# Optimization experiments

Hardware: AMD Instinct MI355X
Metric: run time of the kernel (lower is better)

## Reference

```python
import jax, jax.numpy as jnp
import numpy as np

B, T, N, H, D = 4, 512, 4, 8, 64
FACTOR = 5


def setup_inputs() -> dict:
    key = jax.random.key(0)
    k1, k2, k3, k4 = jax.random.split(key, 4)
    queries = jax.random.normal(k1, (B, T, N, H, D), dtype=jnp.float32)
    keys = jax.random.normal(k2, (B, T, N, H, D), dtype=jnp.float32)
    values = jax.random.normal(k3, (B, T, N, H, D), dtype=jnp.float32)
    sample_k = min(FACTOR * int(np.ceil(np.log(T))), T)  # = 35
    index_sample = jax.random.randint(k4, (T, sample_k), 0, T)
    return {"queries": queries, "keys": keys, "values": values,
            "index_sample": index_sample}


def _merge_heads(x):
    # [B, T, N, H, D] -> [B, H, T, N*D]  (matches transpose(3,2).reshape.transpose(2,1))
    b, t, n, h, d = x.shape
    return jnp.transpose(x, (0, 1, 3, 2, 4)).reshape(b, t, h, n * d).transpose(0, 2, 1, 3)


def reference(queries, keys, values, index_sample):
    b, t, n, h, d = queries.shape
    e = n * d
    Q = _merge_heads(queries)   # [B, H, T, E]
    K = _merge_heads(keys)
    V = _merge_heads(values)
    u = index_sample.shape[1]   # sample_k == n_top == factor*ceil(ln T)

    # --- _prob_QK: sampled QK scores, sparsity measure, top-u query select ---
    K_sample = K[:, :, index_sample, :]                      # [B, H, T, u, E]
    QK_sample = jnp.einsum('bhte,bhtse->bhts', Q, K_sample)  # [B, H, T, u]
    M = QK_sample.max(axis=-1) - QK_sample.sum(axis=-1) / t  # [B, H, T]
    _, M_top = jax.lax.top_k(M, u)                           # [B, H, u]
    Q_reduce = jnp.take_along_axis(Q, M_top[..., None], axis=2)  # [B, H, u, E]
    scores = jnp.einsum('bhue,bhte->bhut', Q_reduce, K)      # [B, H, u, T]

    # scale uses 1/sqrt(d_k) of the ORIGINAL query last dim (D), not N*D
    scores = scores * (1.0 / jnp.sqrt(jnp.asarray(d, scores.dtype)))

    # --- initial context (mask_flag=False): mean of V broadcast over T ---
    context = jnp.broadcast_to(V.mean(axis=2, keepdims=True), (b, h, t, e))

    # --- update context at selected query positions ---
    attn = jax.nn.softmax(scores, axis=-1)                   # [B, H, u, T]
    update = jnp.einsum('bhut,bhte->bhue', attn, V)          # [B, H, u, E]
    bi = jnp.arange(b)[:, None, None]
    hi = jnp.arange(h)[None, :, None]
    context = context.at[bi, hi, M_top].set(update)          # scatter-write

    # [B, H, T, E] -> [B, T, N, H, D]
    out = context.transpose(0, 2, 1, 3).reshape(b, t, h, n, d).transpose(0, 1, 3, 2, 4)
    return out
```

## Files before the change

kernel.cpp:

```cpp
#include <hip/hip_runtime.h>
#include <stdint.h>

#define BB 4
#define TT 512
#define NN 4
#define HH 8
#define DD 64
#define EE 256
#define ROWS 2048
#define UPAD 36
#define NCH 8
#define CH 64


__global__ __launch_bounds__(256)
void m_vmean_kernel(const float* __restrict__ q, const float* __restrict__ k,
                    const float* __restrict__ v, const int* __restrict__ idx,
                    float* __restrict__ M, float* __restrict__ vpart, int U) {
    if (blockIdx.x >= 4096) {
        int blk = blockIdx.x - 4096;
        int chunk = blk & 7, bh = blk >> 3;
        int b = bh >> 3, h = bh & 7;
        int e = threadIdx.x;
        int n = e >> 6, d = e & 63;
        size_t base = (size_t)b * TT * ROWS + (size_t)(n * HH + h) * DD + d;
        float acc = 0.f;
        int t0 = chunk * 64;
        for (int t = t0; t < t0 + 64; ++t)
            acc += v[base + (size_t)t * ROWS];
        vpart[blk * EE + e] = acc;
        return;
    }
    __shared__ int sidx[4][40];
    int wave = threadIdx.x >> 6, lane = threadIdx.x & 63;
    int xcd = blockIdx.x & 7;
    int bh = (xcd << 2) | ((blockIdx.x >> 3) & 3);
    int t = ((blockIdx.x >> 5) << 2) + wave;
    int b = bh >> 3, h = bh & 7;
    if (lane < U) sidx[wave][lane] = idx[t * U + lane] & (TT - 1);
    int g = lane >> 4, x = lane & 15;
    int n = x >> 2;
    int dbase = (x & 3) << 4;
    size_t colbase = (size_t)(n * HH + h) * DD + dbase;
    const float* qr = q + ((size_t)(b * TT + t)) * ROWS + colbase;
    float4 qv0 = *(const float4*)qr;
    float4 qv1 = *(const float4*)(qr + 4);
    float4 qv2 = *(const float4*)(qr + 8);
    float4 qv3 = *(const float4*)(qr + 12);
    float mx = -3.4e38f, sm = 0.f;
    const int NB = (U + 3) >> 2;
    int sP = g; if (sP >= U) sP = U - 1;
    const float* kr = k + ((size_t)(b * TT + sidx[wave][sP])) * ROWS + colbase;
    float4 c0 = *(const float4*)kr,       c1 = *(const float4*)(kr + 4),
           c2 = *(const float4*)(kr + 8), c3 = *(const float4*)(kr + 12);
    for (int bs = 0; bs < NB; ++bs) {
        int sn = ((bs + 1) << 2) + g;
        if (sn >= U) sn = U - 1;
        const float* krn = k + ((size_t)(b * TT + sidx[wave][sn])) * ROWS + colbase;
        float4 n0 = *(const float4*)krn,       n1 = *(const float4*)(krn + 4),
               n2 = *(const float4*)(krn + 8), n3 = *(const float4*)(krn + 12);
        float dot = qv0.x * c0.x + qv0.y * c0.y + qv0.z * c0.z + qv0.w * c0.w
                  + qv1.x * c1.x + qv1.y * c1.y + qv1.z * c1.z + qv1.w * c1.w
                  + qv2.x * c2.x + qv2.y * c2.y + qv2.z * c2.z + qv2.w * c2.w
                  + qv3.x * c3.x + qv3.y * c3.y + qv3.z * c3.z + qv3.w * c3.w;
        #pragma unroll
        for (int off = 1; off < 16; off <<= 1)
            dot += __shfl_xor(dot, off, 64);
        int s = (bs << 2) + g;
        if (s < U) { mx = fmaxf(mx, dot); sm += dot; }
        c0 = n0; c1 = n1; c2 = n2; c3 = n3;
    }
    mx = fmaxf(mx, __shfl_xor(mx, 16, 64));
    mx = fmaxf(mx, __shfl_xor(mx, 32, 64));
    sm += __shfl_xor(sm, 16, 64);
    sm += __shfl_xor(sm, 32, 64);
    if (lane == 0) M[(bh << 9) + t] = mx - sm * (1.0f / TT);
}

__global__ void topk_kernel(const float* __restrict__ M,
                            int* __restrict__ Mtop,
                            const float* __restrict__ vpart,
                            float* __restrict__ vmean, int U) {
    __shared__ float sM[TT];
    int bh = blockIdx.x;
    int t = threadIdx.x;
    sM[t] = M[bh * TT + t];
    if (t < 64) Mtop[bh * 64 + t] = 0;
    if (t < EE) {
        float acc = 0.f;
        #pragma unroll
        for (int c = 0; c < 8; ++c)
            acc += vpart[(bh * 8 + c) * EE + t];
        vmean[bh * EE + t] = acc * (1.0f / TT);
    }
    __syncthreads();
    float mv = sM[t];
    int rank = 0;
    for (int i = 0; i < TT; ++i) {
        float o = sM[i];
        rank += (o > mv) || (o == mv && i < t);
    }
    if (rank < U) Mtop[bh * 64 + rank] = t;
}

__global__ __launch_bounds__(256)
void attn_fill(const float* __restrict__ q, const float* __restrict__ k,
               const float* __restrict__ v, const int* __restrict__ Mtop,
               const float* __restrict__ vmean, float* __restrict__ out,
               float* __restrict__ Opart, float* __restrict__ ml, int U) {
    __shared__ float qs[UPAD * 130];
    __shared__ float Bs[CH * 132];
    __shared__ float S[UPAD * 68];

    if (blockIdx.x >= 256) {
        int fb = blockIdx.x - 256;
        size_t i0 = (size_t)fb * 256 + threadIdx.x;
        #pragma unroll
        for (int r = 0; r < 8; ++r) {
            size_t tid4 = (i0 + (size_t)r * 131072) << 2;
            int d = tid4 & 63;
            size_t rest = tid4 >> 6;
            int h = rest & 7;  rest >>= 3;
            int nn = rest & 3; rest >>= 2;
            int b = (int)(rest >> 9);
            int e = (nn << 6) + d;
            int bh = (b << 3) + h;
            float4 val = *(const float4*)(vmean + (size_t)bh * EE + e);
            *(float4*)(out + tid4) = val;
        }
        return;
    }

    int bx = blockIdx.x;
    int bh = bx >> 3, ch = bx & 7;
    int b = bh >> 3, h = bh & 7;
    int tid = threadIdx.x;
    int wv = tid >> 6, l = tid & 63;

    float acc[4][4];
    #pragma unroll
    for (int i = 0; i < 4; ++i)
        #pragma unroll
        for (int j = 0; j < 4; ++j) acc[i][j] = 0.f;

    for (int h2 = 0; h2 < 2; ++h2) {
        int eb = h2 * 128;
        for (int u = wv; u < UPAD; u += 4) {
            int uu = (u < U) ? u : (U - 1);
            int qt = Mtop[bh * 64 + uu] & (TT - 1);
            size_t rowq = ((size_t)(b * TT + qt)) * ROWS;
            #pragma unroll
            for (int j = 0; j < 2; ++j) {
                int e = eb + l + 64 * j;
                qs[u * 130 + l + 64 * j] = q[rowq + (size_t)((e >> 6) * HH + h) * DD + (e & 63)];
            }
        }
        for (int r = wv; r < CH; r += 4) {
            size_t rowk = ((size_t)(b * TT + ch * CH + r)) * ROWS;
            #pragma unroll
            for (int j = 0; j < 2; ++j) {
                int e = eb + l + 64 * j;
                Bs[r * 129 + l + 64 * j] = k[rowk + (size_t)((e >> 6) * HH + h) * DD + (e & 63)];
            }
        }
        __syncthreads();
        if (tid < 144) {
            int ug = tid >> 4, tg = tid & 15;
            int u0 = ug << 2, t0 = tg << 2;
            for (int e = 0; e < 128; ++e) {
                float kx0 = Bs[(t0 + 0) * 129 + e];
                float kx1 = Bs[(t0 + 1) * 129 + e];
                float kx2 = Bs[(t0 + 2) * 129 + e];
                float kx3 = Bs[(t0 + 3) * 129 + e];
                #pragma unroll
                for (int i = 0; i < 4; ++i) {
                    float qv = qs[(u0 + i) * 130 + e];
                    acc[i][0] += qv * kx0;
                    acc[i][1] += qv * kx1;
                    acc[i][2] += qv * kx2;
                    acc[i][3] += qv * kx3;
                }
            }
        }
        __syncthreads();
    }
    if (tid < 144) {
        int ug = tid >> 4, tg = tid & 15;
        int u0 = ug << 2, t0 = tg << 2;
        #pragma unroll
        for (int i = 0; i < 4; ++i)
            #pragma unroll
            for (int j = 0; j < 4; ++j)
                S[(u0 + i) * 68 + t0 + j] = acc[i][j] * 0.125f;
    }
    __syncthreads();

    if (tid < UPAD) {
        float m = -3.4e38f;
        for (int t = 0; t < CH; ++t) m = fmaxf(m, S[tid * 68 + t]);
        float lsum = 0.f;
        for (int t = 0; t < CH; ++t) {
            float p = __expf(S[tid * 68 + t] - m);
            S[tid * 68 + t] = p;
            lsum += p;
        }
        size_t mli = ((size_t)(bh * NCH + ch) * UPAD + tid) * 2;
        ml[mli] = m;
        ml[mli + 1] = lsum;
    }
    __syncthreads();

    int ugp = tid >> 5, el = tid & 31;
    int u0p = ugp * 5;
    for (int vh = 0; vh < 2; ++vh) {
        for (int r = wv; r < CH; r += 4) {
            size_t rowv = ((size_t)(b * TT + ch * CH + r)) * ROWS;
            #pragma unroll
            for (int j = 0; j < 2; ++j) {
                int e = vh * 128 + l + 64 * j;
                Bs[r * 132 + l + 64 * j] = v[rowv + (size_t)((e >> 6) * HH + h) * DD + (e & 63)];
            }
        }
        __syncthreads();
        float4 o[5];
        #pragma unroll
        for (int i = 0; i < 5; ++i) o[i] = make_float4(0.f, 0.f, 0.f, 0.f);
        for (int t = 0; t < CH; ++t) {
            float4 v4 = *(const float4*)&Bs[t * 132 + 4 * el];
            #pragma unroll
            for (int i = 0; i < 5; ++i) {
                int uc = u0p + i; if (uc > 35) uc = 35;
                float p = S[uc * 68 + t];
                o[i].x += p * v4.x; o[i].y += p * v4.y;
                o[i].z += p * v4.z; o[i].w += p * v4.w;
            }
        }
        #pragma unroll
        for (int i = 0; i < 5; ++i) {
            int u = u0p + i;
            if (u < UPAD)
                *(float4*)&Opart[((size_t)(bh * NCH + ch) * UPAD + u) * EE + vh * 128 + 4 * el] = o[i];
        }
        __syncthreads();
    }
}

__global__ void combine_kernel(const float* __restrict__ Opart,
                               const float* __restrict__ ml,
                               const int* __restrict__ Mtop,
                               float* __restrict__ out, int U) {
    int bx = blockIdx.x;
    int bh = bx / U, ui = bx % U;
    int b = bh >> 3, h = bh & 7;
    int el = threadIdx.x;
    float mc[NCH], lc[NCH];
    float gm = -3.4e38f;
    #pragma unroll
    for (int c = 0; c < NCH; ++c) {
        size_t mli = ((size_t)(bh * NCH + c) * UPAD + ui) * 2;
        mc[c] = ml[mli]; lc[c] = ml[mli + 1];
        gm = fmaxf(gm, mc[c]);
    }
    float L = 0.f;
    float fc[NCH];
    #pragma unroll
    for (int c = 0; c < NCH; ++c) { fc[c] = __expf(mc[c] - gm); L += lc[c] * fc[c]; }
    float inv = 1.0f / L;
    float4 a = make_float4(0.f, 0.f, 0.f, 0.f);
    #pragma unroll
    for (int c = 0; c < NCH; ++c) {
        float4 o = *(const float4*)&Opart[((size_t)(bh * NCH + c) * UPAD + ui) * EE + 4 * el];
        a.x += fc[c] * o.x; a.y += fc[c] * o.y;
        a.z += fc[c] * o.z; a.w += fc[c] * o.w;
    }
    int qt = Mtop[bh * 64 + ui] & (TT - 1);
    int e0 = 4 * el, n = el >> 4;
    size_t ooff = ((size_t)(b * TT + qt)) * ROWS + (size_t)(n * HH + h) * DD + (e0 & 63);
    a.x *= inv; a.y *= inv; a.z *= inv; a.w *= inv;
    *(float4*)(out + ooff) = a;
}


__global__ __launch_bounds__(1024)
void vmean_kernel(const float* __restrict__ v, float* __restrict__ vmean) {
    __shared__ float part[4][EE];
    int bh = blockIdx.x;
    int b = bh >> 3, h = bh & 7;
    int e = threadIdx.x & 255;
    int chunk = threadIdx.x >> 8;
    int n = e >> 6, d = e & 63;
    size_t base = (size_t)b * TT * ROWS + (size_t)(n * HH + h) * DD + d;
    float acc = 0.f;
    int t0 = chunk * 128;
    for (int t = t0; t < t0 + 128; ++t)
        acc += v[base + (size_t)t * ROWS];
    part[chunk][e] = acc;
    __syncthreads();
    if (threadIdx.x < EE)
        vmean[bh * EE + threadIdx.x] =
            (part[0][threadIdx.x] + part[1][threadIdx.x] +
             part[2][threadIdx.x] + part[3][threadIdx.x]) * (1.0f / TT);
}

__global__ void fill_kernel(const float* __restrict__ vmean,
                            float* __restrict__ out) {
    size_t tid4 = ((size_t)blockIdx.x * 256 + threadIdx.x) << 2;
    int d = tid4 & 63;
    size_t rest = tid4 >> 6;
    int h = rest & 7;  rest >>= 3;
    int n = rest & 3;  rest >>= 2;
    int b = (int)(rest >> 9);
    int e = (n << 6) + d;
    int bh = (b << 3) + h;
    float4 val = *(const float4*)(vmean + (size_t)bh * EE + e);
    *(float4*)(out + tid4) = val;
}

__global__ void m_only_kernel(const float* __restrict__ q,
                              const float* __restrict__ k,
                              const int* __restrict__ idx,
                              float* __restrict__ M, int U) {
    int wave = threadIdx.x >> 6, lane = threadIdx.x & 63;
    int r = (blockIdx.x << 2) + wave;
    int t = r & (TT - 1);
    int bh = r >> 9;
    int b = bh >> 3, h = bh & 7;
    int g = lane >> 4, x = lane & 15;
    int n = x >> 2;
    int dbase = (x & 3) << 4;
    size_t colbase = (size_t)(n * HH + h) * DD + dbase;
    size_t qrow = ((size_t)(b * TT + t)) * ROWS + colbase;
    float4 qv0 = *(const float4*)(q + qrow);
    float4 qv1 = *(const float4*)(q + qrow + 4);
    float4 qv2 = *(const float4*)(q + qrow + 8);
    float4 qv3 = *(const float4*)(q + qrow + 12);
    float mx = -3.4e38f, sm = 0.f;
    int NB = (U + 3) >> 2;
    for (int bs = 0; bs < NB; ++bs) {
        int s = (bs << 2) + g;
        int valid = s < U;
        int sc = valid ? s : (U - 1);
        int kt = idx[t * U + sc] & (TT - 1);
        size_t krow = ((size_t)(b * TT + kt)) * ROWS + colbase;
        float4 kv0 = *(const float4*)(k + krow);
        float4 kv1 = *(const float4*)(k + krow + 4);
        float4 kv2 = *(const float4*)(k + krow + 8);
        float4 kv3 = *(const float4*)(k + krow + 12);
        float dot = qv0.x * kv0.x + qv0.y * kv0.y + qv0.z * kv0.z + qv0.w * kv0.w
                  + qv1.x * kv1.x + qv1.y * kv1.y + qv1.z * kv1.z + qv1.w * kv1.w
                  + qv2.x * kv2.x + qv2.y * kv2.y + qv2.z * kv2.z + qv2.w * kv2.w
                  + qv3.x * kv3.x + qv3.y * kv3.y + qv3.z * kv3.z + qv3.w * kv3.w;
        #pragma unroll
        for (int off = 1; off < 16; off <<= 1)
            dot += __shfl_xor(dot, off, 64);
        if (valid) { mx = fmaxf(mx, dot); sm += dot; }
    }
    mx = fmaxf(mx, __shfl_xor(mx, 16, 64));
    mx = fmaxf(mx, __shfl_xor(mx, 32, 64));
    sm += __shfl_xor(sm, 16, 64);
    sm += __shfl_xor(sm, 32, 64);
    if (lane == 0) M[r] = mx - sm * (1.0f / TT);
}

__global__ void topk_only_kernel(const float* __restrict__ M,
                                 int* __restrict__ Mtop, int U) {
    __shared__ float sM[TT];
    int bh = blockIdx.x;
    int t = threadIdx.x;
    sM[t] = M[bh * TT + t];
    if (t < 64) Mtop[bh * 64 + t] = 0;
    __syncthreads();
    float mv = sM[t];
    int rank = 0;
    for (int i = 0; i < TT; ++i) {
        float o = sM[i];
        rank += (o > mv) || (o == mv && i < t);
    }
    if (rank < U) Mtop[bh * 64 + rank] = t;
}

__global__ void update_kernel(const float* __restrict__ q,
                              const float* __restrict__ k,
                              const float* __restrict__ v,
                              const int* __restrict__ Mtop,
                              float* __restrict__ out, int U) {
    __shared__ float qs[EE];
    __shared__ float sc[TT];
    __shared__ float red[256];
    int blk = blockIdx.x;
    int ui = blk % U;
    int bh = blk / U;
    int b = bh >> 3, h = bh & 7;
    int tid = threadIdx.x;
    int qt = Mtop[bh * 64 + ui] & (TT - 1);
    {
        int n = tid >> 6, d = tid & 63;
        qs[tid] = q[((size_t)(b * TT + qt)) * ROWS + (size_t)(n * HH + h) * DD + d];
    }
    __syncthreads();
    #pragma unroll
    for (int rep = 0; rep < 2; ++rep) {
        int t = tid + rep * 256;
        size_t kb = ((size_t)(b * TT + t)) * ROWS + (size_t)h * DD;
        float acc = 0.f;
        #pragma unroll
        for (int n = 0; n < NN; ++n) {
            const float* kn = k + kb + (size_t)n * HH * DD;
            #pragma unroll 4
            for (int d4 = 0; d4 < DD; d4 += 4) {
                float4 kv = *(const float4*)(kn + d4);
                int e = n * 64 + d4;
                acc += qs[e] * kv.x + qs[e + 1] * kv.y + qs[e + 2] * kv.z + qs[e + 3] * kv.w;
            }
        }
        sc[t] = acc * 0.125f;
    }
    __syncthreads();
    red[tid] = fmaxf(sc[tid], sc[tid + 256]);
    __syncthreads();
    for (int s = 128; s > 0; s >>= 1) {
        if (tid < s) red[tid] = fmaxf(red[tid], red[tid + s]);
        __syncthreads();
    }
    float mx = red[0];
    __syncthreads();
    float e0 = __expf(sc[tid] - mx);
    float e1 = __expf(sc[tid + 256] - mx);
    sc[tid] = e0; sc[tid + 256] = e1;
    red[tid] = e0 + e1;
    __syncthreads();
    for (int s = 128; s > 0; s >>= 1) {
        if (tid < s) red[tid] += red[tid + s];
        __syncthreads();
    }
    float inv = 1.0f / red[0];
    __syncthreads();
    {
        int n = tid >> 6, d = tid & 63;
        size_t vb = (size_t)b * TT * ROWS + (size_t)(n * HH + h) * DD + d;
        float acc = 0.f;
        for (int t = 0; t < TT; ++t)
            acc += sc[t] * v[vb + (size_t)t * ROWS];
        out[((size_t)(b * TT + qt)) * ROWS + (size_t)(n * HH + h) * DD + d] = acc * inv;
    }
}

__global__ __launch_bounds__(1024)
void fused_probattn(const float* __restrict__ qp, const float* __restrict__ kp,
                    const float* __restrict__ vp, const int* __restrict__ idx,
                    float* __restrict__ out, int U) {
    __shared__ float vmean[EE];
    __shared__ float M[TT];
    __shared__ float sc[TT];
    __shared__ float qs[EE];
    __shared__ float red[64];
    __shared__ int   Mtop[64];
    const int bh = blockIdx.x;
    const int b = bh >> 3, h = bh & 7;
    const int tid = threadIdx.x;
    const int wave = tid >> 6, lane = tid & 63;
    if (tid < EE) {
        int n = tid >> 6, d = tid & 63;
        size_t base = (size_t)b * TT * ROWS + (size_t)(n * HH + h) * DD + d;
        float acc = 0.f;
        for (int t = 0; t < TT; ++t) acc += vp[base + (size_t)t * ROWS];
        vmean[tid] = acc * (1.0f / TT);
    }
    __syncthreads();
    for (int i = tid; i < TT * EE; i += 1024) {
        int t = i >> 8, e = i & 255;
        int n = e >> 6, d = e & 63;
        out[((size_t)(b * TT + t)) * ROWS + (size_t)(n * HH + h) * DD + d] = vmean[e];
    }
    {
        int e = lane << 2;
        int n = e >> 6, d = e & 63;
        size_t ebase = (size_t)(n * HH + h) * DD + d;
        for (int t = wave; t < TT; t += 16) {
            float4 qv = *(const float4*)(qp + ((size_t)(b * TT + t)) * ROWS + ebase);
            float mx = -3.4e38f, sm = 0.f;
            for (int s = 0; s < U; ++s) {
                int kt = idx[t * U + s] & (TT - 1);
                float4 kv = *(const float4*)(kp + ((size_t)(b * TT + kt)) * ROWS + ebase);
                float dot = qv.x * kv.x + qv.y * kv.y + qv.z * kv.z + qv.w * kv.w;
                #pragma unroll
                for (int off = 32; off; off >>= 1) dot += __shfl_xor(dot, off, 64);
                mx = fmaxf(mx, dot);
                sm += dot;
            }
            if (lane == 0) M[t] = mx - sm * (1.0f / TT);
        }
    }
    __syncthreads();
    if (tid < 64) Mtop[tid] = 0;
    __syncthreads();
    if (tid < TT) {
        float mv = M[tid];
        int rank = 0;
        for (int i = 0; i < TT; ++i) {
            float o = M[i];
            rank += (o > mv) || (o == mv && i < tid);
        }
        if (rank < U) Mtop[rank] = tid;
    }
    __syncthreads();
    for (int ui = 0; ui < U; ++ui) {
        int qt = Mtop[ui];
        if (tid < EE) {
            int n = tid >> 6, d = tid & 63;
            qs[tid] = qp[((size_t)(b * TT + qt)) * ROWS + (size_t)(n * HH + h) * DD + d];
        }
        __syncthreads();
        if (tid < TT) {
            float acc = 0.f;
            size_t kb = ((size_t)(b * TT + tid)) * ROWS + (size_t)h * DD;
            for (int n = 0; n < NN; ++n) {
                const float* kn = kp + kb + (size_t)n * HH * DD;
                for (int d = 0; d < DD; ++d) acc += qs[n * 64 + d] * kn[d];
            }
            sc[tid] = acc * 0.125f;
        }
        __syncthreads();
        float val = (tid < TT) ? sc[tid] : -3.4e38f;
        #pragma unroll
        for (int off = 32; off; off >>= 1) val = fmaxf(val, __shfl_xor(val, off, 64));
        if (lane == 0) red[wave] = val;
        __syncthreads();
        if (tid == 0) {
            float m = red[0];
            for (int w = 1; w < 16; ++w) m = fmaxf(m, red[w]);
            red[32] = m;
        }
        __syncthreads();
        float mx = red[32];
        float ev = 0.f;
        if (tid < TT) { ev = __expf(sc[tid] - mx); sc[tid] = ev; }
        __syncthreads();
        float sv = ev;
        #pragma unroll
        for (int off = 32; off; off >>= 1) sv += __shfl_xor(sv, off, 64);
        if (lane == 0) red[wave] = sv;
        __syncthreads();
        if (tid == 0) {
            float s = 0.f;
            for (int w = 0; w < 16; ++w) s += red[w];
            red[32] = s;
        }
        __syncthreads();
        float inv = 1.0f / red[32];
        if (tid < EE) {
            int n = tid >> 6, d = tid & 63;
            size_t vb = (size_t)b * TT * ROWS + (size_t)(n * HH + h) * DD + d;
            float acc = 0.f;
            for (int t = 0; t < TT; ++t) acc += sc[t] * vp[vb + (size_t)t * ROWS];
            out[((size_t)(b * TT + qt)) * ROWS + (size_t)(n * HH + h) * DD + d] = acc * inv;
        }
        __syncthreads();
    }
}

extern "C" void kernel_launch(void* const* d_in, const int* in_sizes, int n_in,
                              void* d_out, int out_size, void* d_ws, size_t ws_size,
                              hipStream_t stream) {
    const float* q = (const float*)d_in[0];
    const float* k = (const float*)d_in[1];
    const float* v = (const float*)d_in[2];
    const int* idx = (const int*)d_in[3];
    float* out = (float*)d_out;
    int U = in_sizes[3] / TT;

    const size_t NEED_FLASH = 204800 + (size_t)32 * NCH * UPAD * EE * 4 + 1024;
    const size_t NEED_MID = 160 * 1024;
    char* ws = (char*)d_ws;
    float* M     = (float*)(ws);
    int*   Mtop  = (int*)  (ws + 65536);
    float* vmean = (float*)(ws + 98304);
    float* ml    = (float*)(ws + 131072);
    float* Opart = (float*)(ws + 204800);
    float* vpart = (float*)(ws + 204800);

    if (ws_size >= NEED_FLASH && U == 35) {
        m_vmean_kernel<<<4096 + 256, 256, 0, stream>>>(q, k, v, idx, M, vpart, U);
        topk_kernel<<<BB * HH, TT, 0, stream>>>(M, Mtop, vpart, vmean, U);
        attn_fill<<<256 + 512, 256, 0, stream>>>(q, k, v, Mtop, vmean, out, Opart, ml, U);
        combine_kernel<<<BB * HH * U, 64, 0, stream>>>(Opart, ml, Mtop, out, U);
    } else if (ws_size >= NEED_MID) {
        vmean_kernel<<<BB * HH, 1024, 0, stream>>>(v, vmean);
        fill_kernel<<<4096, 256, 0, stream>>>(vmean, out);
        m_only_kernel<<<BB * HH * TT / 4, 256, 0, stream>>>(q, k, idx, M, U);
        topk_only_kernel<<<BB * HH, TT, 0, stream>>>(M, Mtop, U);
        update_kernel<<<BB * HH * U, 256, 0, stream>>>(q, k, v, Mtop, out, U);
    } else {
        fused_probattn<<<BB * HH, 1024, 0, stream>>>(q, k, v, idx, out, U);
    }
}
```

Before: 186.5 us.

## Share sampled K rows across all heads per query and vectorize score LDS reads

The sparsity-measure kernel now gives each block one (batch, t) pair and has it cover all 8 heads. Each sampled K row is read once as a contiguous 2048-float row and reduced per head through shared memory, where before a separate wave gathered 256-wide strided slices for each head. This is meant to cut gather traffic and improve coalescing, though the per-head reduction adds shared-memory passes and syncs. In attn_fill, the Q and K shared tiles are re-padded to 132 floats per row so the QK^T inner loop can read them as float4, which cuts the number of LDS instructions. Bank-conflict behaviour may change as a side effect.

```diff
diff --git a/kernel.cpp b/kernel.cpp
--- a/kernel.cpp
+++ b/kernel.cpp
@@ -9,16 +9,17 @@
 #define EE 256
 #define ROWS 2048
 #define UPAD 36
+#define USAMP 35
 #define NCH 8
 #define CH 64
 
 
 __global__ __launch_bounds__(256)
-void m_vmean_kernel(const float* __restrict__ q, const float* __restrict__ k,
-                    const float* __restrict__ v, const int* __restrict__ idx,
-                    float* __restrict__ M, float* __restrict__ vpart, int U) {
-    if (blockIdx.x >= 4096) {
-        int blk = blockIdx.x - 4096;
+void m2_kernel(const float* __restrict__ q, const float* __restrict__ k,
+               const float* __restrict__ v, const int* __restrict__ idx,
+               float* __restrict__ M, float* __restrict__ vpart) {
+    if (blockIdx.x >= 2048) {
+        int blk = blockIdx.x - 2048;
         int chunk = blk & 7, bh = blk >> 3;
         int b = bh >> 3, h = bh & 7;
         int e = threadIdx.x;
@@ -31,50 +32,50 @@
         vpart[blk * EE + e] = acc;
         return;
     }
-    __shared__ int sidx[4][40];
-    int wave = threadIdx.x >> 6, lane = threadIdx.x & 63;
-    int xcd = blockIdx.x & 7;
-    int bh = (xcd << 2) | ((blockIdx.x >> 3) & 3);
-    int t = ((blockIdx.x >> 5) << 2) + wave;
-    int b = bh >> 3, h = bh & 7;
-    if (lane < U) sidx[wave][lane] = idx[t * U + lane] & (TT - 1);
-    int g = lane >> 4, x = lane & 15;
-    int n = x >> 2;
-    int dbase = (x & 3) << 4;
-    size_t colbase = (size_t)(n * HH + h) * DD + dbase;
-    const float* qr = q + ((size_t)(b * TT + t)) * ROWS + colbase;
-    float4 qv0 = *(const float4*)qr;
-    float4 qv1 = *(const float4*)(qr + 4);
-    float4 qv2 = *(const float4*)(qr + 8);
-    float4 qv3 = *(const float4*)(qr + 12);
-    float mx = -3.4e38f, sm = 0.f;
-    const int NB = (U + 3) >> 2;
-    int sP = g; if (sP >= U) sP = U - 1;
-    const float* kr = k + ((size_t)(b * TT + sidx[wave][sP])) * ROWS + colbase;
-    float4 c0 = *(const float4*)kr,       c1 = *(const float4*)(kr + 4),
-           c2 = *(const float4*)(kr + 8), c3 = *(const float4*)(kr + 12);
-    for (int bs = 0; bs < NB; ++bs) {
-        int sn = ((bs + 1) << 2) + g;
-        if (sn >= U) sn = U - 1;
-        const float* krn = k + ((size_t)(b * TT + sidx[wave][sn])) * ROWS + colbase;
-        float4 n0 = *(const float4*)krn,       n1 = *(const float4*)(krn + 4),
-               n2 = *(const float4*)(krn + 8), n3 = *(const float4*)(krn + 12);
-        float dot = qv0.x * c0.x + qv0.y * c0.y + qv0.z * c0.z + qv0.w * c0.w
-                  + qv1.x * c1.x + qv1.y * c1.y + qv1.z * c1.z + qv1.w * c1.w
-                  + qv2.x * c2.x + qv2.y * c2.y + qv2.z * c2.z + qv2.w * c2.w
-                  + qv3.x * c3.x + qv3.y * c3.y + qv3.z * c3.z + qv3.w * c3.w;
-        #pragma unroll
-        for (int off = 1; off < 16; off <<= 1)
-            dot += __shfl_xor(dot, off, 64);
-        int s = (bs << 2) + g;
-        if (s < U) { mx = fmaxf(mx, dot); sm += dot; }
-        c0 = n0; c1 = n1; c2 = n2; c3 = n3;
-    }
-    mx = fmaxf(mx, __shfl_xor(mx, 16, 64));
-    mx = fmaxf(mx, __shfl_xor(mx, 32, 64));
-    sm += __shfl_xor(sm, 16, 64);
-    sm += __shfl_xor(sm, 32, 64);
-    if (lane == 0) M[(bh << 9) + t] = mx - sm * (1.0f / TT);
+    __shared__ float S[USAMP][33];
+    __shared__ float Dh[8][36];
+    int i = blockIdx.x;
+    int xcd = i & 7;
+    int b = xcd >> 1;
+    int t = ((i >> 3) << 1) | (xcd & 1);
+    int tid = threadIdx.x;
+    int wave = tid >> 6, l = tid & 63;
+    int h = (tid >> 3) & 7;
+
+    const float* qr = q + ((size_t)(b * TT + t)) * ROWS + tid * 8;
+    float4 qa = *(const float4*)qr;
+    float4 qb = *(const float4*)(qr + 4);
+
+    const int* irow = idx + t * USAMP;
+    #pragma unroll
+    for (int s = 0; s < USAMP; ++s) {
+        int kt = __builtin_amdgcn_readfirstlane(irow[s]) & (TT - 1);
+        const float* kr = k + ((size_t)(b * TT + kt)) * ROWS + tid * 8;
+        float4 ka = *(const float4*)kr;
+        float4 kb = *(const float4*)(kr + 4);
+        float p = qa.x * ka.x + qa.y * ka.y + qa.z * ka.z + qa.w * ka.w
+                + qb.x * kb.x + qb.y * kb.y + qb.z * kb.z + qb.w * kb.w;
+        p += __shfl_xor(p, 1, 64);
+        p += __shfl_xor(p, 2, 64);
+        p += __shfl_xor(p, 4, 64);
+        if ((l & 7) == 0) S[s][wave * 8 + h] = p;
+    }
+    __syncthreads();
+    for (int j = tid; j < 8 * USAMP; j += 256) {
+        int hh = j / USAMP, s = j - hh * USAMP;
+        Dh[hh][s] = S[s][hh] + S[s][8 + hh] + S[s][16 + hh] + S[s][24 + hh];
+    }
+    __syncthreads();
+    if (tid < 8) {
+        float mx = -3.4e38f, sm = 0.f;
+        #pragma unroll
+        for (int s = 0; s < USAMP; ++s) {
+            float d = Dh[tid][s];
+            mx = fmaxf(mx, d);
+            sm += d;
+        }
+        M[(((b << 3) + tid) << 9) + t] = mx - sm * (1.0f / TT);
+    }
 }
 
 __global__ void topk_kernel(const float* __restrict__ M,
@@ -108,7 +109,7 @@
                const float* __restrict__ v, const int* __restrict__ Mtop,
                const float* __restrict__ vmean, float* __restrict__ out,
                float* __restrict__ Opart, float* __restrict__ ml, int U) {
-    __shared__ float qs[UPAD * 130];
+    __shared__ float qs[UPAD * 132];
     __shared__ float Bs[CH * 132];
     __shared__ float S[UPAD * 68];
 
@@ -152,7 +153,7 @@
             #pragma unroll
             for (int j = 0; j < 2; ++j) {
                 int e = eb + l + 64 * j;
-                qs[u * 130 + l + 64 * j] = q[rowq + (size_t)((e >> 6) * HH + h) * DD + (e & 63)];
+                qs[u * 132 + l + 64 * j] = q[rowq + (size_t)((e >> 6) * HH + h) * DD + (e & 63)];
             }
         }
         for (int r = wv; r < CH; r += 4) {
@@ -160,25 +161,27 @@
             #pragma unroll
             for (int j = 0; j < 2; ++j) {
                 int e = eb + l + 64 * j;
-                Bs[r * 129 + l + 64 * j] = k[rowk + (size_t)((e >> 6) * HH + h) * DD + (e & 63)];
+                Bs[r * 132 + l + 64 * j] = k[rowk + (size_t)((e >> 6) * HH + h) * DD + (e & 63)];
             }
         }
         __syncthreads();
         if (tid < 144) {
             int ug = tid >> 4, tg = tid & 15;
             int u0 = ug << 2, t0 = tg << 2;
-            for (int e = 0; e < 128; ++e) {
-                float kx0 = Bs[(t0 + 0) * 129 + e];
-                float kx1 = Bs[(t0 + 1) * 129 + e];
-                float kx2 = Bs[(t0 + 2) * 129 + e];
-                float kx3 = Bs[(t0 + 3) * 129 + e];
+            const float4* Qv = (const float4*)qs;
+            const float4* Bv = (const float4*)Bs;
+            for (int e4 = 0; e4 < 32; ++e4) {
+                float4 k0 = Bv[(t0 + 0) * 33 + e4];
+                float4 k1 = Bv[(t0 + 1) * 33 + e4];
+                float4 k2 = Bv[(t0 + 2) * 33 + e4];
+                float4 k3 = Bv[(t0 + 3) * 33 + e4];
                 #pragma unroll
                 for (int i = 0; i < 4; ++i) {
-                    float qv = qs[(u0 + i) * 130 + e];
-                    acc[i][0] += qv * kx0;
-                    acc[i][1] += qv * kx1;
-                    acc[i][2] += qv * kx2;
-                    acc[i][3] += qv * kx3;
+                    float4 qv = Qv[(u0 + i) * 33 + e4];
+                    acc[i][0] += qv.x * k0.x + qv.y * k0.y + qv.z * k0.z + qv.w * k0.w;
+                    acc[i][1] += qv.x * k1.x + qv.y * k1.y + qv.z * k1.z + qv.w * k1.w;
+                    acc[i][2] += qv.x * k2.x + qv.y * k2.y + qv.z * k2.z + qv.w * k2.w;
+                    acc[i][3] += qv.x * k3.x + qv.y * k3.y + qv.z * k3.z + qv.w * k3.w;
                 }
             }
         }
@@ -579,8 +582,8 @@
     float* Opart = (float*)(ws + 204800);
     float* vpart = (float*)(ws + 204800);
 
-    if (ws_size >= NEED_FLASH && U == 35) {
-        m_vmean_kernel<<<4096 + 256, 256, 0, stream>>>(q, k, v, idx, M, vpart, U);
+    if (ws_size >= NEED_FLASH && U == USAMP) {
+        m2_kernel<<<2048 + 256, 256, 0, stream>>>(q, k, v, idx, M, vpart);
         topk_kernel<<<BB * HH, TT, 0, stream>>>(M, Mtop, vpart, vmean, U);
         attn_fill<<<256 + 512, 256, 0, stream>>>(q, k, v, Mtop, vmean, out, Opart, ml, U);
         combine_kernel<<<BB * HH * U, 64, 0, stream>>>(Opart, ml, Mtop, out, U);
```

Result: faster. 171.6 us (-8.0%).
